# Performance work log

Measured on AMD Instinct MI355X. Metric: run time of the kernel, lower is better.

## Reference

```python
import jax, jax.numpy as jnp
import numpy as np

D_MODEL = 2048
N_HEADS = 16
HEAD_DIM = D_MODEL // N_HEADS
B, T = 2, 2048


def setup_inputs() -> dict:
    key = jax.random.key(0)
    ks = jax.random.split(key, 7)
    s = 0.02
    return {
        "x": jax.random.normal(ks[0], (B, T, D_MODEL), dtype=jnp.float32),
        "w_qkv": jax.random.normal(ks[1], (D_MODEL, 3 * D_MODEL), dtype=jnp.float32) * s,
        "w_proj": jax.random.normal(ks[2], (D_MODEL, D_MODEL), dtype=jnp.float32) * s,
        "w_ff1": jax.random.normal(ks[3], (D_MODEL, 4 * D_MODEL), dtype=jnp.float32) * s,
        "b_ff1": jnp.zeros((4 * D_MODEL,), dtype=jnp.float32),
        "w_ff2": jax.random.normal(ks[4], (4 * D_MODEL, D_MODEL), dtype=jnp.float32) * s,
        "b_ff2": jnp.zeros((D_MODEL,), dtype=jnp.float32),
    }


def reference(x, w_qkv, w_proj, w_ff1, b_ff1, w_ff2, b_ff2):
    Bs, Ts, C = x.shape
    H, hd = N_HEADS, HEAD_DIM
    # fused qkv projection
    qkv = jnp.einsum("btc,cd->btd", x, w_qkv)
    q, k, v = jnp.split(qkv, 3, axis=-1)
    # (B, T, C) -> (B, H, T, hd)
    q = q.reshape(Bs, Ts, H, hd).transpose(0, 2, 1, 3)
    k = k.reshape(Bs, Ts, H, hd).transpose(0, 2, 1, 3)
    v = v.reshape(Bs, Ts, H, hd).transpose(0, 2, 1, 3)
    # paged KV write + gather round-trip (empty cache, n_kv_head == n_heads)
    # is the identity on k, v; attention is causal SDPA over the full cache.
    scale = 1.0 / jnp.sqrt(jnp.asarray(hd, dtype=x.dtype))
    scores = jnp.einsum("bhqd,bhkd->bhqk", q, k) * scale
    causal = jnp.tril(jnp.ones((Ts, Ts), dtype=bool))
    scores = jnp.where(causal, scores, jnp.finfo(scores.dtype).min)
    attn = jax.nn.softmax(scores, axis=-1)
    out = jnp.einsum("bhqk,bhkd->bhqd", attn, v)  # (B, H, T, hd)
    out = out.transpose(0, 2, 1, 3).reshape(Bs, Ts, C)
    attn_out = jnp.einsum("btc,cd->btd", out, w_proj)
    # feed-forward with exact GELU (torch nn.GELU default)
    h = jax.nn.gelu(jnp.einsum("btc,cf->btf", x, w_ff1) + b_ff1, approximate=False)
    ff_out = jnp.einsum("btf,fc->btc", h, w_ff2) + b_ff2
    return x + attn_out + ff_out
```

## Files before the change

kernel.cpp:

```cpp
#include <hip/hip_runtime.h>
#include <hip/hip_bf16.h>
#include <cmath>

typedef __bf16 bf16x8 __attribute__((ext_vector_type(8)));
typedef float f32x4 __attribute__((ext_vector_type(4)));
typedef float f32x16 __attribute__((ext_vector_type(16)));
typedef unsigned short u16;
typedef unsigned int u32;

#define DEV __device__ __forceinline__

static constexpr int BB = 2;
static constexpr int T = 2048;
static constexpr int DM = 2048;
static constexpr int NH = 16;
static constexpr int HD = 128;
static constexpr int FF = 8192;
static constexpr int M = BB * T;
static constexpr int NQKV = 3 * DM;

DEV u16 f2b(float f) {
  u32 u = __builtin_bit_cast(u32, f);
  u = (u + 0x7FFFu + ((u >> 16) & 1u)) >> 16;
  return (u16)u;
}
DEV float b2f(u16 h) {
  u32 u = ((u32)h) << 16;
  return __builtin_bit_cast(float, u);
}

DEV void gload16(const u16* g, const u16* l) {
  __builtin_amdgcn_global_load_lds(
      (const __attribute__((address_space(1))) void*)(uintptr_t)g,
      (__attribute__((address_space(3))) void*)(unsigned)(uintptr_t)l,
      16, 0, 0);
}


__global__ void cvt_f32_to_bf16(const float* __restrict__ in, u16* __restrict__ out, int n4) {
  int i = blockIdx.x * blockDim.x + threadIdx.x;
  if (i >= n4) return;
  float4 v = reinterpret_cast<const float4*>(in)[i];
  ushort4 o;
  o.x = f2b(v.x); o.y = f2b(v.y); o.z = f2b(v.z); o.w = f2b(v.w);
  reinterpret_cast<ushort4*>(out)[i] = o;
}

__global__ void transpose_cvt(const float* __restrict__ W, u16* __restrict__ Wt, int K, int N) {
  __shared__ float tile[32][33];
  int nb = blockIdx.x * 32, kb = blockIdx.y * 32;
  int r = threadIdx.x >> 3;
  int c4 = (threadIdx.x & 7) * 4;
  float4 v = *reinterpret_cast<const float4*>(&W[(size_t)(kb + r) * N + nb + c4]);
  tile[r][c4] = v.x; tile[r][c4 + 1] = v.y; tile[r][c4 + 2] = v.z; tile[r][c4 + 3] = v.w;
  __syncthreads();
  ushort4 o;
  o.x = f2b(tile[c4][r]);     o.y = f2b(tile[c4 + 1][r]);
  o.z = f2b(tile[c4 + 2][r]); o.w = f2b(tile[c4 + 3][r]);
  *reinterpret_cast<ushort4*>(&Wt[(size_t)(nb + r) * K + kb + c4]) = o;
}

__global__ void ff2_reduce(const float* __restrict__ p0, const float* __restrict__ p1,
                           const float* __restrict__ bias, const float* __restrict__ x,
                           const u16* __restrict__ ap, float* __restrict__ out) {
  int i = blockIdx.x * blockDim.x + threadIdx.x;
  float4 a = reinterpret_cast<const float4*>(p0)[i];
  float4 b = reinterpret_cast<const float4*>(p1)[i];
  float4 xx = reinterpret_cast<const float4*>(x)[i];
  float4 bi = reinterpret_cast<const float4*>(bias)[i & (DM / 4 - 1)];
  ushort4 a4 = reinterpret_cast<const ushort4*>(ap)[i];
  float4 o;
  o.x = a.x + b.x + bi.x + xx.x + b2f(a4.x);
  o.y = a.y + b.y + bi.y + xx.y + b2f(a4.y);
  o.z = a.z + b.z + bi.z + xx.z + b2f(a4.z);
  o.w = a.w + b.w + bi.w + xx.w + b2f(a4.w);
  reinterpret_cast<float4*>(out)[i] = o;
}

template <int EPI>
__global__ __launch_bounds__(512, 2) void gemm8(
    const u16* __restrict__ A, const u16* __restrict__ Bt, int Ndim,
    int Kstride, int Klen, int gx, int tpp,
    u16* __restrict__ out_bf, float* __restrict__ p0, float* __restrict__ p1,
    const float* __restrict__ bias) {
  __shared__ __align__(16) u16 lds[2 * 32768];
  const int t = threadIdx.x;
  const int nwg = gridDim.x, cpx = nwg >> 3;
  const int wg = (blockIdx.x & 7) * cpx + (blockIdx.x >> 3);
  const int part = wg / tpp, tid = wg % tpp;
  const int m0 = (tid / gx) * 256, n0 = (tid % gx) * 256;
  const int wave = t >> 6, lane = t & 63;
  const int wm = wave >> 2, wn = wave & 3;
  const int lr = lane & 15, lk = lane >> 4;

  const int srow = t >> 3;
  const int sc8 = ((t & 7) ^ (srow & 7)) * 8;
  const u16* gA = &A[(size_t)(m0 + srow) * Kstride + (size_t)part * Klen + sc8];
  const u16* gB = &Bt[(size_t)(n0 + srow) * Kstride + (size_t)part * Klen + sc8];
  const int wls = wave * 512;

  u16* buf0 = lds;
  u16* buf1 = lds + 32768;

#define STAGE_A(buf, h, kt)                                                      \
  {                                                                              \
    gload16(gA + (size_t)((h) * 128) * Kstride + (kt) * 64,                      \
            (buf) + (h) * 8192 + wls);                                           \
    gload16(gA + (size_t)((h) * 128 + 64) * Kstride + (kt) * 64,                 \
            (buf) + (h) * 8192 + 4096 + wls);                                    \
  }
#define STAGE_B(buf, h, kt)                                                      \
  {                                                                              \
    gload16(gB + (size_t)((h) * 128) * Kstride + (kt) * 64,                      \
            (buf) + 16384 + (h) * 8192 + wls);                                   \
    gload16(gB + (size_t)((h) * 128 + 64) * Kstride + (kt) * 64,                 \
            (buf) + 16384 + (h) * 8192 + 4096 + wls);                            \
  }
#define PH_PRE                          \
  __builtin_amdgcn_sched_barrier(0);    \
  __builtin_amdgcn_s_barrier();         \
  __builtin_amdgcn_sched_barrier(0);    \
  __builtin_amdgcn_s_setprio(1);
#define PH_POST                         \
  __builtin_amdgcn_s_setprio(0);        \
  __builtin_amdgcn_sched_barrier(0);    \
  __builtin_amdgcn_s_barrier();         \
  __builtin_amdgcn_sched_barrier(0);

  const int NT = Klen >> 6;

  STAGE_A(buf0, 0, 0); STAGE_A(buf0, 1, 0);
  STAGE_B(buf0, 0, 0); STAGE_B(buf0, 1, 0);
  STAGE_A(buf1, 0, 1); STAGE_B(buf1, 0, 1);
  __builtin_amdgcn_sched_barrier(0);
  asm volatile("s_waitcnt vmcnt(4)" ::: "memory");
  __builtin_amdgcn_s_barrier();
  __builtin_amdgcn_sched_barrier(0);

  f32x4 acc[8][4] = {};
  const int aBase = (wm * 128 + lr) * 64;
  const int bBase = 16384 + (wn * 64 + lr) * 64;
  const int c0 = (lk ^ (lr & 7)) * 8;
  const int c1 = ((4 + lk) ^ (lr & 7)) * 8;

  u16* cur = buf0;
  u16* alt = buf1;
  bf16x8 af[4][2], bq0[2][2], bq1[2][2];

  for (int kt = 0; kt < NT; ++kt) {
#pragma unroll
    for (int i = 0; i < 4; ++i) {
      af[i][0] = *(const bf16x8*)&cur[aBase + i * 1024 + c0];
      af[i][1] = *(const bf16x8*)&cur[aBase + i * 1024 + c1];
    }
#pragma unroll
    for (int j = 0; j < 2; ++j) {
      bq0[j][0] = *(const bf16x8*)&cur[bBase + j * 1024 + c0];
      bq0[j][1] = *(const bf16x8*)&cur[bBase + j * 1024 + c1];
    }
    if (kt + 1 < NT) STAGE_A(alt, 1, kt + 1);
    PH_PRE;
#pragma unroll
    for (int i = 0; i < 4; ++i)
#pragma unroll
      for (int j = 0; j < 2; ++j)
#pragma unroll
        for (int kk = 0; kk < 2; ++kk)
          acc[i][j] = __builtin_amdgcn_mfma_f32_16x16x32_bf16(af[i][kk], bq0[j][kk], acc[i][j], 0, 0, 0);
    PH_POST;
#pragma unroll
    for (int j = 0; j < 2; ++j) {
      bq1[j][0] = *(const bf16x8*)&cur[bBase + (2 + j) * 1024 + c0];
      bq1[j][1] = *(const bf16x8*)&cur[bBase + (2 + j) * 1024 + c1];
    }
    if (kt + 1 < NT) STAGE_B(alt, 1, kt + 1);
    PH_PRE;
#pragma unroll
    for (int i = 0; i < 4; ++i)
#pragma unroll
      for (int j = 0; j < 2; ++j)
#pragma unroll
        for (int kk = 0; kk < 2; ++kk)
          acc[i][2 + j] = __builtin_amdgcn_mfma_f32_16x16x32_bf16(af[i][kk], bq1[j][kk], acc[i][2 + j], 0, 0, 0);
    PH_POST;
#pragma unroll
    for (int i = 0; i < 4; ++i) {
      af[i][0] = *(const bf16x8*)&cur[aBase + (4 + i) * 1024 + c0];
      af[i][1] = *(const bf16x8*)&cur[aBase + (4 + i) * 1024 + c1];
    }
    if (kt + 2 < NT) STAGE_A(cur, 0, kt + 2);
    PH_PRE;
#pragma unroll
    for (int i = 0; i < 4; ++i)
#pragma unroll
      for (int j = 0; j < 2; ++j)
#pragma unroll
        for (int kk = 0; kk < 2; ++kk)
          acc[4 + i][2 + j] = __builtin_amdgcn_mfma_f32_16x16x32_bf16(af[i][kk], bq1[j][kk], acc[4 + i][2 + j], 0, 0, 0);
    PH_POST;
    if (kt + 2 < NT) STAGE_B(cur, 0, kt + 2);
    PH_PRE;
#pragma unroll
    for (int i = 0; i < 4; ++i)
#pragma unroll
      for (int j = 0; j < 2; ++j)
#pragma unroll
        for (int kk = 0; kk < 2; ++kk)
          acc[4 + i][j] = __builtin_amdgcn_mfma_f32_16x16x32_bf16(af[i][kk], bq0[j][kk], acc[4 + i][j], 0, 0, 0);
    __builtin_amdgcn_s_setprio(0);
    __builtin_amdgcn_sched_barrier(0);
    if (kt + 2 < NT)      asm volatile("s_waitcnt vmcnt(4)" ::: "memory");
    else if (kt + 1 < NT) asm volatile("s_waitcnt vmcnt(0)" ::: "memory");
    __builtin_amdgcn_s_barrier();
    __builtin_amdgcn_sched_barrier(0);
    u16* tmp = cur; cur = alt; alt = tmp;
  }
#undef STAGE_A
#undef STAGE_B
#undef PH_PRE
#undef PH_POST

  float* pout = (part == 0) ? p0 : p1;
#pragma unroll
  for (int i = 0; i < 8; ++i) {
#pragma unroll
    for (int j = 0; j < 4; ++j) {
#pragma unroll
      for (int r = 0; r < 4; ++r) {
        int gr = m0 + wm * 128 + i * 16 + (lane >> 4) * 4 + r;
        int gc = n0 + wn * 64 + j * 16 + (lane & 15);
        float v = acc[i][j][r];
        if constexpr (EPI == 0) {
          int part_ = gc >> 11, cc = gc & 2047;
          int head = cc >> 7, d = cc & 127;
          int b = gr >> 11, tt = gr & 2047;
          int bh = b * NH + head;
          size_t addr = (((size_t)(bh * 64 + (tt >> 5)) * 8 + (d >> 4)) * 512)
                        + ((tt & 31) + ((d >> 3) & 1) * 32) * 8 + (d & 7);
          out_bf[(size_t)part_ * M * DM + addr] = f2b(v);
        } else if constexpr (EPI == 2) {
          v += bias[gc];
          float u = v * (v * v * 0.044715f + 1.0f) * 0.7978845608028654f;
          float e = exp2f(u * 2.885390081777927f);
          float th = 1.0f - 2.0f / (e + 1.0f);
          v = 0.5f * v * (1.0f + th);
          out_bf[(size_t)gr * Ndim + gc] = f2b(v);
        } else {
          pout[(size_t)gr * Ndim + gc] = v;
        }
      }
    }
  }
}

template <int EPI>
__global__ __launch_bounds__(512, 4) void gemm_bf16(
    const u16* __restrict__ A, const u16* __restrict__ Bt, int Ndim, int K, int gx,
    u16* __restrict__ out_bf, float* __restrict__ out_f32,
    const float* __restrict__ bias,
    const float* __restrict__ resid_f32, const u16* __restrict__ resid_bf) {
  __shared__ __align__(16) u16 lds[3 * (256 + 128) * 32];
  const int t = threadIdx.x;
  const int nwg = gridDim.x, cpx = nwg >> 3;
  const int wg = (blockIdx.x & 7) * cpx + (blockIdx.x >> 3);
  const int m0 = (wg / gx) * 256, n0 = (wg % gx) * 128;
  const int wave = t >> 6, lane = t & 63;
  const int wm = wave >> 1, wn = wave & 1;
  const int lr = lane & 15, lk = lane >> 4;

  u16* cA = lds;                   u16* cB = lds + 8192;
  u16* nA = lds + 12288;           u16* nB = lds + 12288 + 8192;
  u16* sA = lds + 2 * 12288;       u16* sB = lds + 2 * 12288 + 8192;

  const int sk = ((lane & 3) ^ ((lane >> 3) & 3)) * 8;
  const u16* gA0 = &A[(size_t)(m0 + wave * 16 + (lane >> 2)) * K + sk];
  const u16* gA1 = gA0 + (size_t)128 * K;
  const u16* gB0 = &Bt[(size_t)(n0 + wave * 16 + (lane >> 2)) * K + sk];

  const int wbase = wave * 512;

  auto stage = [&](u16* dA, u16* dB) {
    gload16(gA0, dA + wbase);
    gload16(gA1, dA + 4096 + wbase);
    gload16(gB0, dB + wbase);
    gA0 += 32; gA1 += 32; gB0 += 32;
  };

  const int NT = K >> 5;

  stage(cA, cB);
  stage(nA, nB);
  __builtin_amdgcn_sched_barrier(0);
  asm volatile("s_waitcnt vmcnt(3)" ::: "memory");
  __builtin_amdgcn_s_barrier();
  __builtin_amdgcn_sched_barrier(0);

  f32x4 acc[4][4] = {};
  const int rcol = (lk ^ ((lr >> 1) & 3)) * 8;

  for (int kt = 0; kt < NT; ++kt) {
    if (kt + 2 < NT) stage(sA, sB);
    bf16x8 af[4], bfr[4];
#pragma unroll
    for (int i = 0; i < 4; ++i) {
      af[i]  = *reinterpret_cast<const bf16x8*>(&cA[(wm * 64 + i * 16 + lr) * 32 + rcol]);
      bfr[i] = *reinterpret_cast<const bf16x8*>(&cB[(wn * 64 + i * 16 + lr) * 32 + rcol]);
    }
#pragma unroll
    for (int i = 0; i < 4; ++i)
#pragma unroll
      for (int j = 0; j < 4; ++j)
        acc[i][j] = __builtin_amdgcn_mfma_f32_16x16x32_bf16(af[i], bfr[j], acc[i][j], 0, 0, 0);
    if (kt + 1 < NT) {
      __builtin_amdgcn_sched_barrier(0);
      if (kt + 2 < NT) asm volatile("s_waitcnt vmcnt(3)" ::: "memory");
      else             asm volatile("s_waitcnt vmcnt(0)" ::: "memory");
      __builtin_amdgcn_s_barrier();
      __builtin_amdgcn_sched_barrier(0);
      u16* tA = cA; u16* tB = cB;
      cA = nA; cB = nB; nA = sA; nB = sB; sA = tA; sB = tB;
    }
  }

#pragma unroll
  for (int i = 0; i < 4; ++i) {
#pragma unroll
    for (int j = 0; j < 4; ++j) {
#pragma unroll
      for (int r = 0; r < 4; ++r) {
        int gr = m0 + wm * 64 + i * 16 + (lane >> 4) * 4 + r;
        int gc = n0 + wn * 64 + j * 16 + (lane & 15);
        float v = acc[i][j][r];
        if constexpr (EPI == 1) {
          out_bf[(size_t)gr * Ndim + gc] = f2b(v);
        } else if constexpr (EPI == 3) {
          v += bias[gc] + resid_f32[(size_t)gr * Ndim + gc] + b2f(resid_bf[(size_t)gr * Ndim + gc]);
          out_f32[(size_t)gr * Ndim + gc] = v;
        } else {
          int hh = gr >> 7, d = gr & 127;
          int b = gc >> 11, tt = gc & 2047;
          int bh = b * NH + hh;
          size_t addr = (((size_t)(bh * 128 + (tt >> 4)) * 4 + (d >> 5)) * 512)
                        + ((d & 31) + ((tt >> 3) & 1) * 32) * 8 + (tt & 7);
          out_bf[addr] = f2b(v);
        }
      }
    }
  }
}

__global__ __launch_bounds__(256) void attn_frag(
    const u16* __restrict__ qf_, const u16* __restrict__ kf_,
    const u16* __restrict__ vf_, u16* __restrict__ outg) {
  const int l = threadIdx.x & 63;
  const int wq = threadIdx.x >> 6;
  const int bh = blockIdx.y;
  const int qi = gridDim.x - 1 - blockIdx.x;
  const int qb = qi * 4 + wq;
  const int h = l >> 5, ln = l & 31;
  const int qrow = qb * 32 + ln;

  const u16* qbase = qf_ + ((size_t)(bh * 64 + qb) * 8) * 512 + l * 8;
  bf16x8 qf[8];
#pragma unroll
  for (int s = 0; s < 8; ++s)
    qf[s] = *reinterpret_cast<const bf16x8*>(qbase + s * 512);

  f32x16 acc0 = {}, acc1 = {}, acc2 = {}, acc3 = {};
  float mrow = -INFINITY, lrow = 0.f;
  const float scaleL = 0.08838834764831845f * 1.4426950408889634f;
  const int ntiles = qb + 1;

  for (int kt = 0; kt < ntiles; ++kt) {
    const u16* kbase = kf_ + ((size_t)(bh * 64 + kt) * 8) * 512 + l * 8;
    f32x16 sa = {};
#pragma unroll
    for (int s = 0; s < 8; ++s) {
      bf16x8 kf = *reinterpret_cast<const bf16x8*>(kbase + s * 512);
      sa = __builtin_amdgcn_mfma_f32_32x32x16_bf16(kf, qf[s], sa, 0, 0, 0);
    }

    float p[16];
    float lmax = -INFINITY;
    const bool diag = (kt == qb);
#pragma unroll
    for (int r = 0; r < 16; ++r) {
      float sv = sa[r] * scaleL;
      if (diag) {
        int kv = kt * 32 + (r & 3) + 8 * (r >> 2) + 4 * h;
        if (kv > qrow) sv = -INFINITY;
      }
      p[r] = sv;
      lmax = fmaxf(lmax, sv);
    }
    float rmax = fmaxf(lmax, __shfl_xor(lmax, 32));

    if (__any(rmax > mrow + 11.5f)) {
      float mnew = fmaxf(mrow, rmax);
      float corr = exp2f(mrow - mnew);
      mrow = mnew;
      lrow *= corr;
#pragma unroll
      for (int r = 0; r < 16; ++r) {
        float cr = __shfl(corr, (r & 3) + 8 * (r >> 2) + 4 * h);
        acc0[r] *= cr; acc1[r] *= cr; acc2[r] *= cr; acc3[r] *= cr;
      }
    }

    float ls = 0.f;
#pragma unroll
    for (int r = 0; r < 16; ++r) {
      p[r] = exp2f(p[r] - mrow);
      ls += p[r];
    }
    lrow += ls + __shfl_xor(ls, 32);

    u32 w[8];
#pragma unroll
    for (int c = 0; c < 8; ++c)
      asm("v_cvt_pk_bf16_f32 %0, %1, %2" : "=v"(w[c]) : "v"(p[2 * c]), "v"(p[2 * c + 1]));
    u32 x[8];
#pragma unroll
    for (int c = 0; c < 8; ++c) x[c] = (u32)__shfl_xor((int)w[c], 32);
    uint4 A0, A1;
    A0.x = h ? x[2] : w[0]; A0.y = h ? x[3] : w[1];
    A0.z = h ? w[2] : x[0]; A0.w = h ? w[3] : x[1];
    A1.x = h ? x[6] : w[4]; A1.y = h ? x[7] : w[5];
    A1.z = h ? w[6] : x[4]; A1.w = h ? w[7] : x[5];
    bf16x8 pa0 = __builtin_bit_cast(bf16x8, A0);
    bf16x8 pa1 = __builtin_bit_cast(bf16x8, A1);

    const u16* vbase = vf_ + ((size_t)(bh * 128 + kt * 2) * 4) * 512 + l * 8;
    bf16x8 v0, v1;
    v0 = *reinterpret_cast<const bf16x8*>(vbase + 0 * 512);
    v1 = *reinterpret_cast<const bf16x8*>(vbase + 4 * 512);
    acc0 = __builtin_amdgcn_mfma_f32_32x32x16_bf16(pa0, v0, acc0, 0, 0, 0);
    acc0 = __builtin_amdgcn_mfma_f32_32x32x16_bf16(pa1, v1, acc0, 0, 0, 0);
    v0 = *reinterpret_cast<const bf16x8*>(vbase + 1 * 512);
    v1 = *reinterpret_cast<const bf16x8*>(vbase + 5 * 512);
    acc1 = __builtin_amdgcn_mfma_f32_32x32x16_bf16(pa0, v0, acc1, 0, 0, 0);
    acc1 = __builtin_amdgcn_mfma_f32_32x32x16_bf16(pa1, v1, acc1, 0, 0, 0);
    v0 = *reinterpret_cast<const bf16x8*>(vbase + 2 * 512);
    v1 = *reinterpret_cast<const bf16x8*>(vbase + 6 * 512);
    acc2 = __builtin_amdgcn_mfma_f32_32x32x16_bf16(pa0, v0, acc2, 0, 0, 0);
    acc2 = __builtin_amdgcn_mfma_f32_32x32x16_bf16(pa1, v1, acc2, 0, 0, 0);
    v0 = *reinterpret_cast<const bf16x8*>(vbase + 3 * 512);
    v1 = *reinterpret_cast<const bf16x8*>(vbase + 7 * 512);
    acc3 = __builtin_amdgcn_mfma_f32_32x32x16_bf16(pa0, v0, acc3, 0, 0, 0);
    acc3 = __builtin_amdgcn_mfma_f32_32x32x16_bf16(pa1, v1, acc3, 0, 0, 0);
  }

  const int b = bh >> 4, hh = bh & 15;
#pragma unroll
  for (int r = 0; r < 16; ++r) {
    int qr = (r & 3) + 8 * (r >> 2) + 4 * h;
    float lr = __shfl(lrow, qr);
    float rl = 1.0f / lr;
    int tt = qb * 32 + qr;
    size_t rowoff = ((size_t)(b * T + tt)) * DM + hh * HD + ln;
    outg[rowoff + 0]  = f2b(acc0[r] * rl);
    outg[rowoff + 32] = f2b(acc1[r] * rl);
    outg[rowoff + 64] = f2b(acc2[r] * rl);
    outg[rowoff + 96] = f2b(acc3[r] * rl);
  }
}


extern "C" void kernel_launch(void* const* d_in, const int* in_sizes, int n_in,
                              void* d_out, int out_size, void* d_ws, size_t ws_size,
                              hipStream_t stream) {
  const float* x      = (const float*)d_in[0];
  const float* w_qkv  = (const float*)d_in[1];
  const float* w_proj = (const float*)d_in[2];
  const float* w_ff1  = (const float*)d_in[3];
  const float* b_ff1  = (const float*)d_in[4];
  const float* w_ff2  = (const float*)d_in[5];
  const float* b_ff2  = (const float*)d_in[6];
  float* out = (float*)d_out;

  u16* ws = (u16*)d_ws;
  size_t o = 0;
  u16* x_bf      = ws + o; o += (size_t)M * DM;
  u16* wqkv_t    = ws + o; o += (size_t)NQKV * DM;
  u16* wproj_t   = ws + o; o += (size_t)DM * DM;
  u16* wff1_t    = ws + o; o += (size_t)FF * DM;
  u16* wff2_t    = ws + o; o += (size_t)DM * FF;
  u16* attn_proj = ws + o; o += (size_t)M * DM;
  u16* qbuf      = ws + o;
  u16* kbuf      = qbuf + (size_t)M * DM;
  u16* vtbuf     = kbuf + (size_t)M * DM;
  u16* attn_out  = vtbuf + (size_t)M * DM;
  u16* hbuf      = qbuf;

  float* p0 = (float*)ws;
  float* p1 = (float*)wff1_t;

  cvt_f32_to_bf16<<<(M * DM / 4 + 255) / 256, 256, 0, stream>>>(x, x_bf, M * DM / 4);
  transpose_cvt<<<dim3(NQKV / 32, DM / 32), 256, 0, stream>>>(w_qkv, wqkv_t, DM, NQKV);
  transpose_cvt<<<dim3(DM / 32, DM / 32), 256, 0, stream>>>(w_proj, wproj_t, DM, DM);
  transpose_cvt<<<dim3(FF / 32, DM / 32), 256, 0, stream>>>(w_ff1, wff1_t, DM, FF);
  transpose_cvt<<<dim3(DM / 32, FF / 32), 256, 0, stream>>>(w_ff2, wff2_t, FF, DM);

  gemm8<0><<<256, 512, 0, stream>>>(x_bf, wqkv_t, 4096, DM, DM, 16, 256,
                                    qbuf, nullptr, nullptr, nullptr);

  gemm_bf16<4><<<256, 512, 0, stream>>>(
      wqkv_t + (size_t)4096 * DM, x_bf, M, DM, 32, vtbuf, nullptr, nullptr, nullptr, nullptr);

  attn_frag<<<dim3(T / 128, BB * NH), 256, 0, stream>>>(qbuf, kbuf, vtbuf, attn_out);

  gemm_bf16<1><<<256, 512, 0, stream>>>(
      attn_out, wproj_t, DM, DM, 16, attn_proj, nullptr, nullptr, nullptr, nullptr);

  gemm8<2><<<512, 512, 0, stream>>>(x_bf, wff1_t, FF, DM, DM, 32, 512,
                                    hbuf, nullptr, nullptr, b_ff1);

  gemm8<5><<<256, 512, 0, stream>>>(hbuf, wff2_t, DM, FF, 4096, 8, 128,
                                    nullptr, p0, p1, nullptr);

  ff2_reduce<<<M * DM / 4 / 256, 256, 0, stream>>>(p0, p1, b_ff2, x, attn_proj, out);
}
```

Before: 636.8 us.

## Software-pipeline LDS fragment loads across MFMA phases in GEMM main loop

Restructures the GEMM inner loop so that LDS fragment reads for the next phase are issued after each barrier and overlap the current phase's MFMAs. It keeps separate register sets for both A halves and both B halves, and prefetches the first A/B fragments of the next K-tile at the end of the iteration. The aim is to hide LDS read latency behind matrix math and to drop one barrier per phase. In exchange it raises VGPR pressure from the extra fragment registers, which could hurt occupancy or cause spills.

```diff
diff --git a/kernel.cpp b/kernel.cpp
--- a/kernel.cpp
+++ b/kernel.cpp
@@ -116,13 +116,7 @@
     gload16(gB + (size_t)((h) * 128 + 64) * Kstride + (kt) * 64,                 \
             (buf) + 16384 + (h) * 8192 + 4096 + wls);                            \
   }
-#define PH_PRE                          \
-  __builtin_amdgcn_sched_barrier(0);    \
-  __builtin_amdgcn_s_barrier();         \
-  __builtin_amdgcn_sched_barrier(0);    \
-  __builtin_amdgcn_s_setprio(1);
-#define PH_POST                         \
-  __builtin_amdgcn_s_setprio(0);        \
+#define BARR                            \
   __builtin_amdgcn_sched_barrier(0);    \
   __builtin_amdgcn_s_barrier();         \
   __builtin_amdgcn_sched_barrier(0);
@@ -145,68 +139,73 @@
 
   u16* cur = buf0;
   u16* alt = buf1;
-  bf16x8 af[4][2], bq0[2][2], bq1[2][2];
+  bf16x8 a03[4][2], a47[4][2], b01[2][2], b23[2][2];
+
+#pragma unroll
+  for (int i = 0; i < 4; ++i) {
+    a03[i][0] = *(const bf16x8*)&cur[aBase + i * 1024 + c0];
+    a03[i][1] = *(const bf16x8*)&cur[aBase + i * 1024 + c1];
+  }
+#pragma unroll
+  for (int j = 0; j < 2; ++j) {
+    b01[j][0] = *(const bf16x8*)&cur[bBase + j * 1024 + c0];
+    b01[j][1] = *(const bf16x8*)&cur[bBase + j * 1024 + c1];
+  }
 
   for (int kt = 0; kt < NT; ++kt) {
+    if (kt + 1 < NT) STAGE_A(alt, 1, kt + 1);
+    BARR;
+#pragma unroll
+    for (int j = 0; j < 2; ++j) {
+      b23[j][0] = *(const bf16x8*)&cur[bBase + (2 + j) * 1024 + c0];
+      b23[j][1] = *(const bf16x8*)&cur[bBase + (2 + j) * 1024 + c1];
+    }
+    __builtin_amdgcn_s_setprio(1);
+#pragma unroll
+    for (int i = 0; i < 4; ++i)
+#pragma unroll
+      for (int j = 0; j < 2; ++j)
+#pragma unroll
+        for (int kk = 0; kk < 2; ++kk)
+          acc[i][j] = __builtin_amdgcn_mfma_f32_16x16x32_bf16(a03[i][kk], b01[j][kk], acc[i][j], 0, 0, 0);
+    __builtin_amdgcn_s_setprio(0);
+    if (kt + 1 < NT) STAGE_B(alt, 1, kt + 1);
+    BARR;
 #pragma unroll
     for (int i = 0; i < 4; ++i) {
-      af[i][0] = *(const bf16x8*)&cur[aBase + i * 1024 + c0];
-      af[i][1] = *(const bf16x8*)&cur[aBase + i * 1024 + c1];
-    }
-#pragma unroll
-    for (int j = 0; j < 2; ++j) {
-      bq0[j][0] = *(const bf16x8*)&cur[bBase + j * 1024 + c0];
-      bq0[j][1] = *(const bf16x8*)&cur[bBase + j * 1024 + c1];
-    }
-    if (kt + 1 < NT) STAGE_A(alt, 1, kt + 1);
-    PH_PRE;
+      a47[i][0] = *(const bf16x8*)&cur[aBase + (4 + i) * 1024 + c0];
+      a47[i][1] = *(const bf16x8*)&cur[aBase + (4 + i) * 1024 + c1];
+    }
+    __builtin_amdgcn_s_setprio(1);
 #pragma unroll
     for (int i = 0; i < 4; ++i)
 #pragma unroll
       for (int j = 0; j < 2; ++j)
 #pragma unroll
         for (int kk = 0; kk < 2; ++kk)
-          acc[i][j] = __builtin_amdgcn_mfma_f32_16x16x32_bf16(af[i][kk], bq0[j][kk], acc[i][j], 0, 0, 0);
-    PH_POST;
-#pragma unroll
-    for (int j = 0; j < 2; ++j) {
-      bq1[j][0] = *(const bf16x8*)&cur[bBase + (2 + j) * 1024 + c0];
-      bq1[j][1] = *(const bf16x8*)&cur[bBase + (2 + j) * 1024 + c1];
-    }
-    if (kt + 1 < NT) STAGE_B(alt, 1, kt + 1);
-    PH_PRE;
+          acc[i][2 + j] = __builtin_amdgcn_mfma_f32_16x16x32_bf16(a03[i][kk], b23[j][kk], acc[i][2 + j], 0, 0, 0);
+    __builtin_amdgcn_s_setprio(0);
+    if (kt + 2 < NT) STAGE_A(cur, 0, kt + 2);
+    BARR;
+    __builtin_amdgcn_s_setprio(1);
 #pragma unroll
     for (int i = 0; i < 4; ++i)
 #pragma unroll
       for (int j = 0; j < 2; ++j)
 #pragma unroll
         for (int kk = 0; kk < 2; ++kk)
-          acc[i][2 + j] = __builtin_amdgcn_mfma_f32_16x16x32_bf16(af[i][kk], bq1[j][kk], acc[i][2 + j], 0, 0, 0);
-    PH_POST;
-#pragma unroll
-    for (int i = 0; i < 4; ++i) {
-      af[i][0] = *(const bf16x8*)&cur[aBase + (4 + i) * 1024 + c0];
-      af[i][1] = *(const bf16x8*)&cur[aBase + (4 + i) * 1024 + c1];
-    }
-    if (kt + 2 < NT) STAGE_A(cur, 0, kt + 2);
-    PH_PRE;
+          acc[4 + i][2 + j] = __builtin_amdgcn_mfma_f32_16x16x32_bf16(a47[i][kk], b23[j][kk], acc[4 + i][2 + j], 0, 0, 0);
+    __builtin_amdgcn_s_setprio(0);
+    if (kt + 2 < NT) STAGE_B(cur, 0, kt + 2);
+    BARR;
+    __builtin_amdgcn_s_setprio(1);
 #pragma unroll
     for (int i = 0; i < 4; ++i)
 #pragma unroll
       for (int j = 0; j < 2; ++j)
 #pragma unroll
         for (int kk = 0; kk < 2; ++kk)
-          acc[4 + i][2 + j] = __builtin_amdgcn_mfma_f32_16x16x32_bf16(af[i][kk], bq1[j][kk], acc[4 + i][2 + j], 0, 0, 0);
-    PH_POST;
-    if (kt + 2 < NT) STAGE_B(cur, 0, kt + 2);
-    PH_PRE;
-#pragma unroll
-    for (int i = 0; i < 4; ++i)
-#pragma unroll
-      for (int j = 0; j < 2; ++j)
-#pragma unroll
-        for (int kk = 0; kk < 2; ++kk)
-          acc[4 + i][j] = __builtin_amdgcn_mfma_f32_16x16x32_bf16(af[i][kk], bq0[j][kk], acc[4 + i][j], 0, 0, 0);
+          acc[4 + i][j] = __builtin_amdgcn_mfma_f32_16x16x32_bf16(a47[i][kk], b01[j][kk], acc[4 + i][j], 0, 0, 0);
     __builtin_amdgcn_s_setprio(0);
     __builtin_amdgcn_sched_barrier(0);
     if (kt + 2 < NT)      asm volatile("s_waitcnt vmcnt(4)" ::: "memory");
@@ -214,11 +213,22 @@
     __builtin_amdgcn_s_barrier();
     __builtin_amdgcn_sched_barrier(0);
     u16* tmp = cur; cur = alt; alt = tmp;
+    if (kt + 1 < NT) {
+#pragma unroll
+      for (int i = 0; i < 4; ++i) {
+        a03[i][0] = *(const bf16x8*)&cur[aBase + i * 1024 + c0];
+        a03[i][1] = *(const bf16x8*)&cur[aBase + i * 1024 + c1];
+      }
+#pragma unroll
+      for (int j = 0; j < 2; ++j) {
+        b01[j][0] = *(const bf16x8*)&cur[bBase + j * 1024 + c0];
+        b01[j][1] = *(const bf16x8*)&cur[bBase + j * 1024 + c1];
+      }
+    }
   }
 #undef STAGE_A
 #undef STAGE_B
-#undef PH_PRE
-#undef PH_POST
+#undef BARR
 
   float* pout = (part == 0) ? p0 : p1;
 #pragma unroll
```

Result: no change. 626.3 us (-1.7%).
